# Performance work log

Measured on AMD Instinct MI355X. Metric: run time of the kernel, lower is better.

## Reference

```python
import jax, jax.numpy as jnp
import numpy as np

B, S, H, N = 512, 50, 512, 20000


def setup_inputs() -> dict:
    key = jax.random.key(0)
    ks = jax.random.split(key, 8)
    sc = 1.0 / np.sqrt(H)
    return {
        "all_memory": jax.random.normal(ks[0], (B, S, H), jnp.float32),
        "last_memory": jax.random.normal(ks[1], (B, H), jnp.float32),
        "item_seq": jax.random.randint(ks[2], (B, S), 0, N),
        "mask": jnp.zeros((B, S), dtype=bool),
        "U_w": jax.random.normal(ks[3], (H, H), jnp.float32) * sc,
        "W_w": jax.random.normal(ks[4], (H, H), jnp.float32) * sc,
        "V_w": jax.random.normal(ks[5], (H,), jnp.float32) * sc,
        "V_b": jnp.zeros((1,), jnp.float32),
        "E_w": jax.random.normal(ks[6], (N, 2 * H), jnp.float32) * sc,
    }


def reference(all_memory, last_memory, item_seq, mask, U_w, W_w, V_w, V_b, E_w):
    # Additive (Bahdanau) attention over the basket-sequence memory.
    # torch nn.Linear computes x @ W.T (dropout is identity at eval).
    am = jnp.einsum('bsh,kh->bsk', all_memory, U_w)          # U_explore(all_memory)
    lm = last_memory @ W_w.T                                  # W_explore(last_memory)
    scores = jnp.tanh(am + lm[:, None, :]) @ V_w + V_b[0]     # [B, S]
    scores = jnp.where(mask, -1e9, scores)                    # masked_fill_
    alpha = jax.nn.softmax(scores, axis=1)                    # softmax over seq dim
    ctx = jnp.einsum('bs,bsh->bh', alpha, all_memory)         # attention readout
    feat = jnp.concatenate([ctx, last_memory], axis=-1)       # [B, 2H]
    logits = feat @ E_w.T                                     # [B, N] big GEMM
    # explore_mask = bmm((item_seq>0), one_hot(item_seq)) == scatter-add of counts
    counts = jnp.zeros((B, N), jnp.float32).at[
        jnp.arange(B)[:, None], item_seq
    ].add((item_seq > 0).astype(jnp.float32))
    logits = jnp.where(counts > 0, -jnp.inf, logits)          # mask seen items
    return jax.nn.sigmoid(logits)                             # sigmoid(-inf) -> 0
```

## Files before the change

kernel.cpp:

```cpp
#include <hip/hip_runtime.h>
#include <hip/hip_bf16.h>

#define Bdim 512
#define Sdim 50
#define Hdim 512
#define Ndim 20000
#define Kdim2 1024
#define SEENW 640

typedef __bf16 bf16x8 __attribute__((ext_vector_type(8)));
typedef float f32x4 __attribute__((ext_vector_type(4)));
typedef unsigned short u16;

__device__ __forceinline__ u16 f2bf(float f) {
  unsigned u = __builtin_bit_cast(unsigned, f);
  u = (u + 0x7fffu + ((u >> 16) & 1u)) >> 16;
  return (u16)u;
}
__device__ __forceinline__ float bf2f(u16 v) {
  unsigned u = ((unsigned)v) << 16;
  return __builtin_bit_cast(float, u);
}

__global__ __launch_bounds__(256) void cast2_kernel(const float* __restrict__ a, u16* __restrict__ da, int n4a,
                                                    const float* __restrict__ b, u16* __restrict__ db, int n4b) {
  int stride = gridDim.x * blockDim.x;
  int ntot = n4a + n4b;
  for (int i = blockIdx.x * blockDim.x + threadIdx.x; i < ntot; i += stride) {
    const float4* src; ushort4* dst; int j;
    if (i < n4a) { src = reinterpret_cast<const float4*>(a); dst = reinterpret_cast<ushort4*>(da); j = i; }
    else         { src = reinterpret_cast<const float4*>(b); dst = reinterpret_cast<ushort4*>(db); j = i - n4a; }
    float4 v = src[j];
    ushort4 o;
    o.x = f2bf(v.x); o.y = f2bf(v.y); o.z = f2bf(v.z); o.w = f2bf(v.w);
    dst[j] = o;
  }
}

__global__ __launch_bounds__(256) void prep_kernel(const float* __restrict__ a, u16* __restrict__ da,
                                                   const float* __restrict__ b, u16* __restrict__ db,
                                                   const float* __restrict__ c, u16* __restrict__ dc,
                                                   float* __restrict__ scores, float* __restrict__ lm,
                                                   unsigned* __restrict__ seen) {
  int i = blockIdx.x * blockDim.x + threadIdx.x;
  float4 v; ushort4 o;
  v = reinterpret_cast<const float4*>(a)[i];
  o.x = f2bf(v.x); o.y = f2bf(v.y); o.z = f2bf(v.z); o.w = f2bf(v.w);
  reinterpret_cast<ushort4*>(da)[i] = o;
  v = reinterpret_cast<const float4*>(b)[i];
  o.x = f2bf(v.x); o.y = f2bf(v.y); o.z = f2bf(v.z); o.w = f2bf(v.w);
  reinterpret_cast<ushort4*>(db)[i] = o;
  v = reinterpret_cast<const float4*>(c)[i];
  o.x = f2bf(v.x); o.y = f2bf(v.y); o.z = f2bf(v.z); o.w = f2bf(v.w);
  reinterpret_cast<ushort4*>(dc)[i] = o;
  int stride = gridDim.x * blockDim.x;
  for (int j = i; j < Bdim * Sdim; j += stride) scores[j] = 0.f;
  for (int j = i; j < Bdim * Hdim; j += stride) lm[j] = 0.f;
  for (int j = i; j < Bdim * SEENW; j += stride) seen[j] = 0u;
}

__global__ __launch_bounds__(256) void scatter_kernel(const int* __restrict__ iseq,
                                                      unsigned* __restrict__ seen) {
  int i = blockIdx.x * blockDim.x + threadIdx.x;
  if (i < Bdim * Sdim) {
    int b = i / Sdim;
    int it = iseq[i];
    if (it > 0) atomicOr(&seen[b * SEENW + (it >> 5)], 1u << (it & 31));
  }
}

__global__ __launch_bounds__(256) void softmax_ctx_kernel(
    const float* __restrict__ scores, const unsigned char* __restrict__ mask,
    const u16* __restrict__ amB, const float* __restrict__ last_memory,
    u16* __restrict__ feat) {
  int b = blockIdx.x;
  __shared__ float alpha[Sdim];
  int tid = threadIdx.x;
  if (tid < 64) {
    float s = -1e30f;
    if (tid < Sdim) {
      s = scores[b * Sdim + tid];
      if (mask[b * Sdim + tid]) s = -1e9f;
    }
    float m = s;
#pragma unroll
    for (int off = 32; off; off >>= 1) m = fmaxf(m, __shfl_xor(m, off));
    float e = (tid < Sdim) ? __expf(s - m) : 0.f;
    float sum = e;
#pragma unroll
    for (int off = 32; off; off >>= 1) sum += __shfl_xor(sum, off);
    if (tid < Sdim) alpha[tid] = e / sum;
  }
  __syncthreads();
  for (int h = tid; h < Hdim; h += 256) {
    const u16* amp = amB + ((long)b * Sdim) * Hdim + h;
    float c = 0.f;
#pragma unroll 5
    for (int s = 0; s < Sdim; ++s) c += alpha[s] * bf2f(amp[(long)s * Hdim]);
    feat[b * Kdim2 + h] = f2bf(c);
    feat[b * Kdim2 + Hdim + h] = f2bf(last_memory[b * Hdim + h]);
  }
}

#define BM 256
#define BN 128
#define BK 32

template <int EPI>
__global__ __launch_bounds__(512, 4) void gemm_bt(
    const u16* __restrict__ A, const u16* __restrict__ Bmat,
    int M, int N, int K,
    float* __restrict__ out,
    const float* __restrict__ lm, const float* __restrict__ Vw,
    float* __restrict__ scores, const unsigned* __restrict__ seen) {
  __shared__ bf16x8 Asl[2][BM * BK / 8];
  __shared__ bf16x8 Bsl[2][BN * BK / 8];
  const int tid = threadIdx.x;
  const int lane = tid & 63;
  const int wid = tid >> 6;
  const int wr = wid >> 1, wc = wid & 1;
  const int la = lane & 15, lb = lane >> 4;

  int bx, by, kt0, kt1;
  if constexpr (EPI == 0) {
    bx = blockIdx.x; by = blockIdx.y;
    int ktotal = K / BK; int kper = ktotal / gridDim.z;
    kt0 = blockIdx.z * kper; kt1 = kt0 + kper;
  } else {
    int nwg = gridDim.x, bid = blockIdx.x;
    int q = nwg >> 3, r = nwg & 7;
    int x = bid & 7, i = bid >> 3;
    int wgid = (x < r ? x * (q + 1) : r * (q + 1) + (x - r) * q) + i;
    if constexpr (EPI == 1) { by = wgid >> 2; bx = wgid & 3; }
    else                    { bx = wgid >> 1; by = wgid & 1; }
    kt0 = 0; kt1 = K / BK;
  }
  const int m0 = by * BM;
  const int n0 = bx * BN;

  f32x4 acc[4][4];
  const f32x4 zero = {0.f, 0.f, 0.f, 0.f};
#pragma unroll
  for (int i = 0; i < 4; ++i)
#pragma unroll
    for (int j = 0; j < 4; ++j) acc[i][j] = zero;

  const int rA0 = tid >> 2, eA = (tid & 3) * 8;
  const int rA1 = 128 + (tid >> 2);
  int brB = n0 + (tid >> 2); if (brB > N - 1) brB = N - 1;
  const u16* gA0 = A + (long)(m0 + rA0) * K + eA;
  const u16* gA1 = A + (long)(m0 + rA1) * K + eA;
  const u16* gB  = Bmat + (long)brB * K + eA;

  auto STAGE = [&](int buf, int kt) {
    const int k0 = kt * BK;
    __builtin_amdgcn_global_load_lds((const __attribute__((address_space(1))) void*)(gA0 + k0),
                                     (__attribute__((address_space(3))) void*)(void*)&Asl[buf][wid * 64], 16, 0, 0);
    __builtin_amdgcn_global_load_lds((const __attribute__((address_space(1))) void*)(gA1 + k0),
                                     (__attribute__((address_space(3))) void*)(void*)&Asl[buf][512 + wid * 64], 16, 0, 0);
    __builtin_amdgcn_global_load_lds((const __attribute__((address_space(1))) void*)(gB + k0),
                                     (__attribute__((address_space(3))) void*)(void*)&Bsl[buf][wid * 64], 16, 0, 0);
  };

  STAGE(0, kt0);
  __syncthreads();
  int cur = 0;
  for (int kt = kt0; kt < kt1; ++kt) {
    if (kt + 1 < kt1) STAGE(cur ^ 1, kt + 1);

    bf16x8 af[4], bfr[4];
#pragma unroll
    for (int mi = 0; mi < 4; ++mi)
      af[mi] = Asl[cur][(wr * 64 + mi * 16 + la) * 4 + lb];
#pragma unroll
    for (int ni = 0; ni < 4; ++ni)
      bfr[ni] = Bsl[cur][(wc * 64 + ni * 16 + la) * 4 + lb];
#pragma unroll
    for (int mi = 0; mi < 4; ++mi)
#pragma unroll
      for (int ni = 0; ni < 4; ++ni)
        acc[mi][ni] = __builtin_amdgcn_mfma_f32_16x16x32_bf16(af[mi], bfr[ni], acc[mi][ni], 0, 0, 0);
    __syncthreads();
    cur ^= 1;
  }

  if constexpr (EPI == 0) {
#pragma unroll
    for (int mi = 0; mi < 4; ++mi)
#pragma unroll
      for (int i = 0; i < 4; ++i) {
        int r = m0 + wr * 64 + mi * 16 + lb * 4 + i;
#pragma unroll
        for (int ni = 0; ni < 4; ++ni) {
          int c = n0 + wc * 64 + ni * 16 + la;
          atomicAdd(&out[(long)r * N + c], acc[mi][ni][i]);
        }
      }
  }
  if constexpr (EPI == 1) {
#pragma unroll
    for (int mi = 0; mi < 4; ++mi)
#pragma unroll
      for (int i = 0; i < 4; ++i) {
        int r = m0 + wr * 64 + mi * 16 + lb * 4 + i;
        int bidx = r / Sdim;
        float p = 0.f;
#pragma unroll
        for (int ni = 0; ni < 4; ++ni) {
          int c = n0 + wc * 64 + ni * 16 + la;
          float x = acc[mi][ni][i] + lm[bidx * Hdim + c];
          x = fminf(fmaxf(x, -9.f), 9.f);
          float e = __expf(2.f * x);
          p += Vw[c] * ((e - 1.f) / (e + 1.f));
        }
        p += __shfl_xor(p, 1);
        p += __shfl_xor(p, 2);
        p += __shfl_xor(p, 4);
        p += __shfl_xor(p, 8);
        if (la == 0) atomicAdd(&scores[r], p);
      }
  }
  if constexpr (EPI == 2) {
#pragma unroll
    for (int mi = 0; mi < 4; ++mi)
#pragma unroll
      for (int i = 0; i < 4; ++i) {
        int r = m0 + wr * 64 + mi * 16 + lb * 4 + i;
        long rb = (long)r * Ndim;
#pragma unroll
        for (int ni = 0; ni < 4; ++ni) {
          int c = n0 + wc * 64 + ni * 16 + la;
          if (c < Ndim) {
            unsigned wbits = seen[r * SEENW + (c >> 5)];
            float val = 0.f;
            if (!((wbits >> (c & 31)) & 1u))
              val = 1.f / (1.f + __expf(-acc[mi][ni][i]));
            out[rb + c] = val;
          }
        }
      }
  }
}

extern "C" void kernel_launch(void* const* d_in, const int* in_sizes, int n_in,
                              void* d_out, int out_size, void* d_ws, size_t ws_size,
                              hipStream_t stream) {
  (void)in_sizes; (void)n_in; (void)out_size; (void)ws_size;
  const float* all_memory  = (const float*)d_in[0];
  const float* last_memory = (const float*)d_in[1];
  const int*   item_seq    = (const int*)d_in[2];
  const unsigned char* mask = (const unsigned char*)d_in[3];
  const float* U_w = (const float*)d_in[4];
  const float* W_w = (const float*)d_in[5];
  const float* V_w = (const float*)d_in[6];
  const float* E_w = (const float*)d_in[8];
  float* out = (float*)d_out;

  char* w = (char*)d_ws;
  u16* wsE    = (u16*)w; w += (size_t)Ndim * Kdim2 * 2;
  u16* wsA    = (u16*)w; w += (size_t)Bdim * Sdim * Hdim * 2;
  u16* wsFeat = (u16*)w; w += (size_t)Bdim * Kdim2 * 2;
  u16* wsLast = (u16*)w; w += (size_t)Hdim * Hdim * 2;
  u16* wsW    = (u16*)w; w += (size_t)Hdim * Hdim * 2;
  u16* wsU    = (u16*)w; w += (size_t)Hdim * Hdim * 2;
  float* wsLm     = (float*)w; w += (size_t)Bdim * Hdim * 4;
  float* wsScores = (float*)w; w += (size_t)Bdim * Sdim * 4;
  unsigned* wsSeen = (unsigned*)w; w += (size_t)Bdim * SEENW * 4;

  prep_kernel<<<256, 256, 0, stream>>>(last_memory, wsLast, W_w, wsW, U_w, wsU,
                                       wsScores, wsLm, wsSeen);
  scatter_kernel<<<100, 256, 0, stream>>>(item_seq, wsSeen);
  cast2_kernel<<<4096, 256, 0, stream>>>(E_w, wsE, Ndim * Kdim2 / 4,
                                         all_memory, wsA, Bdim * Sdim * Hdim / 4);

  gemm_bt<0><<<dim3(Hdim / BN, Bdim / BM, 4), 512, 0, stream>>>(
      wsLast, wsW, Bdim, Hdim, Hdim, wsLm, nullptr, nullptr, nullptr, nullptr);
  gemm_bt<1><<<dim3((Bdim * Sdim / BM) * (Hdim / BN)), 512, 0, stream>>>(
      wsA, wsU, Bdim * Sdim, Hdim, Hdim, nullptr, wsLm, V_w, wsScores, nullptr);
  softmax_ctx_kernel<<<Bdim, 256, 0, stream>>>(wsScores, mask, wsA, last_memory, wsFeat);
  gemm_bt<2><<<dim3(((Ndim + BN - 1) / BN) * (Bdim / BM)), 512, 0, stream>>>(
      wsFeat, wsE, Bdim, Ndim, Kdim2, out, nullptr, nullptr, nullptr, wsSeen);
}
```

Baseline: 141.3 us.

## Fuse fp32-to-bf16 conversion of E_w and all_memory into GEMM tile loads

```diff
diff --git a/kernel.cpp b/kernel.cpp
--- a/kernel.cpp
+++ b/kernel.cpp
@@ -21,20 +21,18 @@
   unsigned u = ((unsigned)v) << 16;
   return __builtin_bit_cast(float, u);
 }
-
-__global__ __launch_bounds__(256) void cast2_kernel(const float* __restrict__ a, u16* __restrict__ da, int n4a,
-                                                    const float* __restrict__ b, u16* __restrict__ db, int n4b) {
-  int stride = gridDim.x * blockDim.x;
-  int ntot = n4a + n4b;
-  for (int i = blockIdx.x * blockDim.x + threadIdx.x; i < ntot; i += stride) {
-    const float4* src; ushort4* dst; int j;
-    if (i < n4a) { src = reinterpret_cast<const float4*>(a); dst = reinterpret_cast<ushort4*>(da); j = i; }
-    else         { src = reinterpret_cast<const float4*>(b); dst = reinterpret_cast<ushort4*>(db); j = i - n4a; }
-    float4 v = src[j];
-    ushort4 o;
-    o.x = f2bf(v.x); o.y = f2bf(v.y); o.z = f2bf(v.z); o.w = f2bf(v.w);
-    dst[j] = o;
-  }
+__device__ __forceinline__ unsigned cvt_pk_bf16(float lo, float hi) {
+  unsigned r;
+  asm("v_cvt_pk_bf16_f32 %0, %1, %2" : "=v"(r) : "v"(lo), "v"(hi));
+  return r;
+}
+__device__ __forceinline__ bf16x8 pack8(float4 lo, float4 hi) {
+  union { unsigned u[4]; bf16x8 v; } r;
+  r.u[0] = cvt_pk_bf16(lo.x, lo.y);
+  r.u[1] = cvt_pk_bf16(lo.z, lo.w);
+  r.u[2] = cvt_pk_bf16(hi.x, hi.y);
+  r.u[3] = cvt_pk_bf16(hi.z, hi.w);
+  return r.v;
 }
 
 __global__ __launch_bounds__(256) void prep_kernel(const float* __restrict__ a, u16* __restrict__ da,
@@ -71,7 +69,7 @@
 
 __global__ __launch_bounds__(256) void softmax_ctx_kernel(
     const float* __restrict__ scores, const unsigned char* __restrict__ mask,
-    const u16* __restrict__ amB, const float* __restrict__ last_memory,
+    const float* __restrict__ amF, const float* __restrict__ last_memory,
     u16* __restrict__ feat) {
   int b = blockIdx.x;
   __shared__ float alpha[Sdim];
@@ -93,10 +91,10 @@
   }
   __syncthreads();
   for (int h = tid; h < Hdim; h += 256) {
-    const u16* amp = amB + ((long)b * Sdim) * Hdim + h;
+    const float* amp = amF + ((long)b * Sdim) * Hdim + h;
     float c = 0.f;
 #pragma unroll 5
-    for (int s = 0; s < Sdim; ++s) c += alpha[s] * bf2f(amp[(long)s * Hdim]);
+    for (int s = 0; s < Sdim; ++s) c += alpha[s] * amp[(long)s * Hdim];
     feat[b * Kdim2 + h] = f2bf(c);
     feat[b * Kdim2 + Hdim + h] = f2bf(last_memory[b * Hdim + h]);
   }
@@ -109,6 +107,7 @@
 template <int EPI>
 __global__ __launch_bounds__(512, 4) void gemm_bt(
     const u16* __restrict__ A, const u16* __restrict__ Bmat,
+    const float* __restrict__ Af, const float* __restrict__ Bf,
     int M, int N, int K,
     float* __restrict__ out,
     const float* __restrict__ lm, const float* __restrict__ Vw,
@@ -145,28 +144,73 @@
 #pragma unroll
     for (int j = 0; j < 4; ++j) acc[i][j] = zero;
 
-  const int rA0 = tid >> 2, eA = (tid & 3) * 8;
-  const int rA1 = 128 + (tid >> 2);
-  int brB = n0 + (tid >> 2); if (brB > N - 1) brB = N - 1;
-  const u16* gA0 = A + (long)(m0 + rA0) * K + eA;
-  const u16* gA1 = A + (long)(m0 + rA1) * K + eA;
-  const u16* gB  = Bmat + (long)brB * K + eA;
-
-  auto STAGE = [&](int buf, int kt) {
+  const int rw = tid >> 2;
+  const int eA = (tid & 3) * 8;
+  const int ch = tid & 3;
+  int brB = n0 + rw; if (brB > N - 1) brB = N - 1;
+
+  const u16 *gA0 = nullptr, *gA1 = nullptr, *gB = nullptr;
+  const float *gAf0 = nullptr, *gAf1 = nullptr, *gBf = nullptr;
+  if constexpr (EPI == 1) {
+    gAf0 = Af + (long)(m0 + rw) * K + eA;
+    gAf1 = Af + (long)(m0 + 128 + rw) * K + eA;
+  } else {
+    gA0 = A + (long)(m0 + rw) * K + eA;
+    gA1 = A + (long)(m0 + 128 + rw) * K + eA;
+  }
+  if constexpr (EPI == 2) {
+    gBf = Bf + (long)brB * K + eA;
+  } else {
+    gB = Bmat + (long)brB * K + eA;
+  }
+
+  float4 ra0, ra1, ra2, ra3;
+  float4 rb0, rb1;
+
+  auto STAGE_G = [&](int buf, int kt) {
     const int k0 = kt * BK;
-    __builtin_amdgcn_global_load_lds((const __attribute__((address_space(1))) void*)(gA0 + k0),
-                                     (__attribute__((address_space(3))) void*)(void*)&Asl[buf][wid * 64], 16, 0, 0);
-    __builtin_amdgcn_global_load_lds((const __attribute__((address_space(1))) void*)(gA1 + k0),
-                                     (__attribute__((address_space(3))) void*)(void*)&Asl[buf][512 + wid * 64], 16, 0, 0);
-    __builtin_amdgcn_global_load_lds((const __attribute__((address_space(1))) void*)(gB + k0),
-                                     (__attribute__((address_space(3))) void*)(void*)&Bsl[buf][wid * 64], 16, 0, 0);
+    if constexpr (EPI != 1) {
+      __builtin_amdgcn_global_load_lds((const __attribute__((address_space(1))) void*)(gA0 + k0),
+                                       (__attribute__((address_space(3))) void*)(void*)&Asl[buf][wid * 64], 16, 0, 0);
+      __builtin_amdgcn_global_load_lds((const __attribute__((address_space(1))) void*)(gA1 + k0),
+                                       (__attribute__((address_space(3))) void*)(void*)&Asl[buf][512 + wid * 64], 16, 0, 0);
+    }
+    if constexpr (EPI != 2) {
+      __builtin_amdgcn_global_load_lds((const __attribute__((address_space(1))) void*)(gB + k0),
+                                       (__attribute__((address_space(3))) void*)(void*)&Bsl[buf][wid * 64], 16, 0, 0);
+    }
   };
-
-  STAGE(0, kt0);
+  auto LOADR = [&](int kt) {
+    const int k0 = kt * BK;
+    if constexpr (EPI == 1) {
+      ra0 = *reinterpret_cast<const float4*>(gAf0 + k0);
+      ra1 = *reinterpret_cast<const float4*>(gAf0 + k0 + 4);
+      ra2 = *reinterpret_cast<const float4*>(gAf1 + k0);
+      ra3 = *reinterpret_cast<const float4*>(gAf1 + k0 + 4);
+    }
+    if constexpr (EPI == 2) {
+      rb0 = *reinterpret_cast<const float4*>(gBf + k0);
+      rb1 = *reinterpret_cast<const float4*>(gBf + k0 + 4);
+    }
+  };
+  auto WRITER = [&](int buf) {
+    if constexpr (EPI == 1) {
+      Asl[buf][rw * 4 + ch] = pack8(ra0, ra1);
+      Asl[buf][(128 + rw) * 4 + ch] = pack8(ra2, ra3);
+    }
+    if constexpr (EPI == 2) {
+      Bsl[buf][rw * 4 + ch] = pack8(rb0, rb1);
+    }
+  };
+
+  STAGE_G(0, kt0);
+  LOADR(kt0);
+  WRITER(0);
   __syncthreads();
   int cur = 0;
   for (int kt = kt0; kt < kt1; ++kt) {
-    if (kt + 1 < kt1) STAGE(cur ^ 1, kt + 1);
+    const bool pf = (kt + 1 < kt1);
+    if (pf) { STAGE_G(cur ^ 1, kt + 1); LOADR(kt + 1); }
 
     bf16x8 af[4], bfr[4];
 #pragma unroll
@@ -180,6 +224,8 @@
 #pragma unroll
       for (int ni = 0; ni < 4; ++ni)
         acc[mi][ni] = __builtin_amdgcn_mfma_f32_16x16x32_bf16(af[mi], bfr[ni], acc[mi][ni], 0, 0, 0);
+
+    if (pf) WRITER(cur ^ 1);
     __syncthreads();
     cur ^= 1;
   }
@@ -257,8 +303,6 @@
   float* out = (float*)d_out;
 
   char* w = (char*)d_ws;
-  u16* wsE    = (u16*)w; w += (size_t)Ndim * Kdim2 * 2;
-  u16* wsA    = (u16*)w; w += (size_t)Bdim * Sdim * Hdim * 2;
   u16* wsFeat = (u16*)w; w += (size_t)Bdim * Kdim2 * 2;
   u16* wsLast = (u16*)w; w += (size_t)Hdim * Hdim * 2;
   u16* wsW    = (u16*)w; w += (size_t)Hdim * Hdim * 2;
@@ -270,14 +314,15 @@
   prep_kernel<<<256, 256, 0, stream>>>(last_memory, wsLast, W_w, wsW, U_w, wsU,
                                        wsScores, wsLm, wsSeen);
   scatter_kernel<<<100, 256, 0, stream>>>(item_seq, wsSeen);
-  cast2_kernel<<<4096, 256, 0, stream>>>(E_w, wsE, Ndim * Kdim2 / 4,
-                                         all_memory, wsA, Bdim * Sdim * Hdim / 4);
 
   gemm_bt<0><<<dim3(Hdim / BN, Bdim / BM, 4), 512, 0, stream>>>(
-      wsLast, wsW, Bdim, Hdim, Hdim, wsLm, nullptr, nullptr, nullptr, nullptr);
+      wsLast, wsW, nullptr, nullptr, Bdim, Hdim, Hdim, wsLm,
+      nullptr, nullptr, nullptr, nullptr);
   gemm_bt<1><<<dim3((Bdim * Sdim / BM) * (Hdim / BN)), 512, 0, stream>>>(
-      wsA, wsU, Bdim * Sdim, Hdim, Hdim, nullptr, wsLm, V_w, wsScores, nullptr);
-  softmax_ctx_kernel<<<Bdim, 256, 0, stream>>>(wsScores, mask, wsA, last_memory, wsFeat);
+      nullptr, wsU, all_memory, nullptr, Bdim * Sdim, Hdim, Hdim, nullptr,
+      wsLm, V_w, wsScores, nullptr);
+  softmax_ctx_kernel<<<Bdim, 256, 0, stream>>>(wsScores, mask, all_memory, last_memory, wsFeat);
   gemm_bt<2><<<dim3(((Ndim + BN - 1) / BN) * (Bdim / BM)), 512, 0, stream>>>(
-      wsFeat, wsE, Bdim, Ndim, Kdim2, out, nullptr, nullptr, nullptr, wsSeen);
-}
+      wsFeat, nullptr, nullptr, E_w, Bdim, Ndim, Kdim2, out,
+      nullptr, nullptr, nullptr, wsSeen);
+}
```

Measured after the change: 131.7 us. 1.07x faster.
